# Kernel tuning notes

Hardware: AMD Instinct MI355X
Metric: run time of the kernel (lower is better)

The kernel has to match this reference:

```python
import jax, jax.numpy as jnp
import numpy as np

C_IN = 4
C_OUT = 8
K = 5            # kernel_size (hardcoded by reshape(25,2) in original)
N_ROT = 8
R_B = 8          # rot_basis_size
STRIDE = 1
PAD = 2
TWO_PI = 2.0 * np.pi
ROT_SCALE = TWO_PI / R_B


def B2(x):
    # quadratic B-spline, exactly as in the torch source
    return (-3 * (-0.5 + x) ** 2 * jnp.sign(0.5 - x)
            + (-1.5 + x) ** 2 * jnp.sign(1.5 - x)
            - 3 * (1 + 2 * x) ** 2 * jnp.sign(0.5 + x) / 4
            + (3 + 2 * x) ** 2 * jnp.sign(1.5 + x) / 4) / 4


def angle_dist(th1, th2):
    return jnp.mod(th2 - th1 + np.pi, TWO_PI) - np.pi


def make_kernel_stack(weights):
    # weights: (C_IN, R_B*K*K, C_OUT). M = K*K*R_B combined (spatial-center, rot-center) index;
    # original repeats each spatial center R_B times (np.repeat) and tiles rot centers K*K times.
    lidx = -(K // 2)
    coords = jnp.arange(lidx, K // 2 + 1, dtype=jnp.float32)
    grid = jnp.stack(jnp.meshgrid(coords, coords, indexing='ij'), axis=-1)  # (K,K,2), grid[i,j]=[i+l, j+l]
    centers_xy = jnp.repeat(grid.reshape(K * K, 2), R_B, axis=0)            # (M,2)
    rot_centers = jnp.tile(jnp.arange(R_B, dtype=jnp.float32) * ROT_SCALE, K * K)  # (M,)
    rot_sample = jnp.arange(N_ROT, dtype=jnp.float32) * (TWO_PI / N_ROT)    # (N_ROT,)

    def one_kernel(theta):
        c, s = jnp.cos(theta), jnp.sin(theta)
        x, y = grid[..., 0], grid[..., 1]
        xxs = jnp.stack([x * c - y * s, x * s + y * c], axis=-1)            # (K,K,2) rotated sample grid
        xx_diffs = centers_xy[None, None, :, :] - xxs[:, :, None, :]        # (K,K,M,2)
        xx_vals = jnp.prod(B2(xx_diffs), axis=-1)                           # (K,K,M) separable spatial spline
        rots = rot_sample + theta                                           # (N_ROT,)
        rot_vals = B2(angle_dist(rots[:, None], rot_centers[None, :]) / ROT_SCALE)  # (N_ROT,M)
        vals = xx_vals[:, :, None, :] * rot_vals[None, None, :, :]          # (K,K,N_ROT,M)
        # contract basis index m against weights -> (C_OUT, C_IN, N_ROT, K, K)
        return jnp.einsum('xyrm,imo->oirxy', vals, weights)

    ks = jax.vmap(one_kernel)(-rot_sample)  # (N_ROT, C_OUT, C_IN, N_ROT, K, K), matches torch.cat over -theta
    return ks.reshape(N_ROT * C_OUT, C_IN * N_ROT, K, K)


def setup_inputs() -> dict:
    key = jax.random.key(0)
    kx, kw = jax.random.split(key)
    X = jax.random.normal(kx, (8, C_IN, N_ROT, 256, 256), dtype=jnp.float32)
    weights = jax.random.normal(kw, (C_IN, R_B * K * K, C_OUT), dtype=jnp.float32)
    return {'X': X, 'weights': weights}


def reference(X, weights):
    ks = make_kernel_stack(weights)                       # (N_ROT*C_OUT, C_IN*N_ROT, K, K)
    B, c, d, H, W = X.shape
    Xr = X.reshape(B, c * d, H, W)
    out = jax.lax.conv_general_dilated(
        Xr, ks, window_strides=(STRIDE, STRIDE),
        padding=[(PAD, PAD), (PAD, PAD)],
        dimension_numbers=('NCHW', 'OIHW', 'NCHW'))        # (B, N_ROT*C_OUT, h, w)
    Bn, _, h, w = out.shape
    out = out.reshape(Bn, N_ROT, C_OUT, h, w).transpose(0, 2, 1, 3, 4)  # (B, C_OUT, N_ROT, h, w)
    return (TWO_PI / N_ROT) * out
```

## Files before the change

### kernel.cpp

```cpp
#include <hip/hip_runtime.h>
#include <hip/hip_fp16.h>
#include <math.h>

#define PI_F      3.14159265358979323846f
#define TWO_PI_F  6.28318530717958647692f
#define PI4_F     0.78539816339744830962f

typedef _Float16 f16x8 __attribute__((ext_vector_type(8)));
typedef float    f32x4 __attribute__((ext_vector_type(4)));

__device__ __forceinline__ float sgn(float t) {
    return (t > 0.f) ? 1.f : ((t < 0.f) ? -1.f : 0.f);
}

__device__ __forceinline__ float b2(float x) {
    float a = x - 0.5f;
    float b = x - 1.5f;
    float c = 1.f + 2.f * x;
    float d = 3.f + 2.f * x;
    return (-3.f * a * a * sgn(0.5f - x)
            + b * b * sgn(1.5f - x)
            - 0.75f * c * c * sgn(0.5f + x)
            + 0.25f * d * d * sgn(1.5f + x)) * 0.25f;
}

__global__ void build_ks_kernel(const float* __restrict__ w, __half* __restrict__ ksh) {
    int g = blockIdx.x * 256 + threadIdx.x;
    if (g >= 64 * 32 * 25) return;
    int O = g & 63;
    int rest = g >> 6;
    int t = rest % 25;
    int I = rest / 25;
    int r0 = O >> 3, o = O & 7;
    int i = I >> 3, r = I & 7;
    int x = t / 5, y = t % 5;

    float theta = -(float)r0 * PI4_F;
    float cth = cosf(theta), sth = sinf(theta);
    float fx = (float)(x - 2), fy = (float)(y - 2);
    float xc = fx * cth - fy * sth;
    float yc = fx * sth + fy * cth;

    float rotv[8];
    float rs = (float)r * PI4_F + theta;
    #pragma unroll
    for (int mr = 0; mr < 8; ++mr) {
        float v = (float)mr * PI4_F - rs + PI_F;
        float md = fmodf(v, TWO_PI_F);
        if (md < 0.f) md += TWO_PI_F;
        rotv[mr] = b2((md - PI_F) / PI4_F);
    }

    float sum = 0.f;
    for (int mx = 0; mx < 25; ++mx) {
        float cx = (float)(mx / 5 - 2);
        float cy = (float)(mx % 5 - 2);
        float bx = b2(cx - xc) * b2(cy - yc);
        if (bx != 0.f) {
            const float* wp = w + (size_t)(i * 200 + mx * 8) * 8 + o;
            #pragma unroll
            for (int mr = 0; mr < 8; ++mr)
                sum = fmaf(bx * rotv[mr], wp[mr * 8], sum);
        }
    }
    ksh[(size_t)(t * 64 + O) * 32 + I] = __float2half(sum);
}

__global__ __launch_bounds__(512, 4) void conv_kernel(const float* __restrict__ X,
                                                      const __half* __restrict__ ksh,
                                                      float* __restrict__ out) {
    __shared__ uint4 xt[720 * 5];

    int blk = blockIdx.x;
    int b = blk >> 7;
    int rem = blk & 127;
    int h0 = (rem >> 3) << 4;
    int w0 = (rem & 7) << 5;
    int tid = threadIdx.x;

    const float* Xb = X + (size_t)b * 32 * 65536;

    for (int lin = tid; lin < 2880; lin += 512) {
        int slot = lin / 720;
        int pxi = lin - slot * 720;
        int r = pxi / 36;
        int c = pxi - r * 36;
        int gh = h0 + r - 2;
        int gw = w0 + c - 2;
        union { __half h[8]; uint4 u; } pk;
        if ((unsigned)gh < 256u && (unsigned)gw < 256u) {
            const float* src = Xb + (size_t)slot * 8 * 65536 + gh * 256 + gw;
            #pragma unroll
            for (int j = 0; j < 8; ++j) pk.h[j] = __float2half(src[j * 65536]);
        } else {
            pk.u = make_uint4(0u, 0u, 0u, 0u);
        }
        xt[pxi * 5 + slot] = pk.u;
    }
    __syncthreads();

    int wave = tid >> 6;
    int lane = tid & 63;
    int lO = lane & 15;
    int ks4 = lane >> 4;

    const uint4* ksq = (const uint4*)ksh;
    int bidx = lO * 4 + ks4;

    f32x4 acc[4][4] = {};

    int baseA[4];
    #pragma unroll
    for (int q = 0; q < 4; ++q) {
        int r_q = wave * 2 + (q >> 1);
        int half_q = q & 1;
        baseA[q] = (r_q * 36 + half_q * 16 + lO) * 5 + ks4;
    }

    f16x8 Bf[2][4];
    #pragma unroll
    for (int n = 0; n < 4; ++n)
        Bf[0][n] = __builtin_bit_cast(f16x8, ksq[0 * 256 + n * 64 + bidx]);

    #pragma unroll
    for (int t = 0; t < 25; ++t) {
        const int dx = t / 5, dy = t % 5;
        const int aoff = (dx * 36 + dy) * 5;
        const int cur = t & 1, nxt = cur ^ 1;

        f16x8 Af[4];
        #pragma unroll
        for (int q = 0; q < 4; ++q)
            Af[q] = __builtin_bit_cast(f16x8, xt[baseA[q] + aoff]);

        if (t < 24) {
            #pragma unroll
            for (int n = 0; n < 4; ++n)
                Bf[nxt][n] = __builtin_bit_cast(f16x8, ksq[(t + 1) * 256 + n * 64 + bidx]);
        }

        #pragma unroll
        for (int q = 0; q < 4; ++q) {
            #pragma unroll
            for (int n = 0; n < 4; ++n)
                acc[q][n] = __builtin_amdgcn_mfma_f32_16x16x32_f16(Af[q], Bf[cur][n], acc[q][n], 0, 0, 0);
        }
    }

    #pragma unroll
    for (int q = 0; q < 4; ++q) {
        int r_q = wave * 2 + (q >> 1);
        int gh = h0 + r_q;
        int gwb = w0 + (q & 1) * 16 + ks4 * 4;
        #pragma unroll
        for (int n = 0; n < 4; ++n) {
            int O = n * 16 + lO;
            float* op = out + (((size_t)(b * 8 + (O & 7)) * 8 + (O >> 3)) << 16)
                            + gh * 256 + gwb;
            f32x4 v = acc[q][n] * PI4_F;
            *(f32x4*)op = v;
        }
    }
}

extern "C" void kernel_launch(void* const* d_in, const int* in_sizes, int n_in,
                              void* d_out, int out_size, void* d_ws, size_t ws_size,
                              hipStream_t stream) {
    const float* X = (const float*)d_in[0];
    const float* w = (const float*)d_in[1];
    float* outp = (float*)d_out;
    __half* ksh = (__half*)d_ws;

    build_ks_kernel<<<(64 * 32 * 25 + 255) / 256, 256, 0, stream>>>(w, ksh);
    conv_kernel<<<8 * 16 * 8, 512, 0, stream>>>(X, ksh, outp);
}
```

Measured before the change: 110.6 us.

## Pre-transpose input to fp16 channels-last and stream tiles via async LDS loads

Adds a pass that converts X from fp32 NCHW to an fp16 pixel-major layout with 32 channels contiguous, stored in workspace. A new conv kernel then pulls halo tiles with global_load_lds 16-byte copies, uses a zero guard buffer for padding, and double-buffers four column sub-tiles per block while raising MFMA wave priority. The intent is to replace the strided per-channel fp32 gathers with contiguous async loads overlapped with compute. The cost is an extra full read/write pass over the input and a grid of only 256 single-occupancy blocks; the old path is kept as a fallback when workspace is too small.

```diff
diff --git a/kernel.cpp b/kernel.cpp
--- a/kernel.cpp
+++ b/kernel.cpp
@@ -8,6 +8,11 @@
 
 typedef _Float16 f16x8 __attribute__((ext_vector_type(8)));
 typedef float    f32x4 __attribute__((ext_vector_type(4)));
+
+#define KS_BYTES   (25 * 64 * 32 * 2)
+#define GUARD_OFF  KS_BYTES
+#define XH_OFF     ((size_t)1 << 20)
+#define XH_BYTES   ((size_t)8 * 256 * 256 * 32 * 2)
 
 __device__ __forceinline__ float sgn(float t) {
     return (t > 0.f) ? 1.f : ((t < 0.f) ? -1.f : 0.f);
@@ -24,7 +29,9 @@
             + 0.25f * d * d * sgn(1.5f + x)) * 0.25f;
 }
 
-__global__ void build_ks_kernel(const float* __restrict__ w, __half* __restrict__ ksh) {
+__global__ void build_ks_kernel(const float* __restrict__ w, __half* __restrict__ ksh,
+                                float* __restrict__ guard) {
+    if (blockIdx.x == 0 && threadIdx.x < 16) guard[threadIdx.x] = 0.f;
     int g = blockIdx.x * 256 + threadIdx.x;
     if (g >= 64 * 32 * 25) return;
     int O = g & 63;
@@ -66,99 +73,210 @@
     ksh[(size_t)(t * 64 + O) * 32 + I] = __float2half(sum);
 }
 
-__global__ __launch_bounds__(512, 4) void conv_kernel(const float* __restrict__ X,
-                                                      const __half* __restrict__ ksh,
-                                                      float* __restrict__ out) {
+__global__ __launch_bounds__(256, 2) void hwc_kernel(const float* __restrict__ X,
+                                                     __half* __restrict__ Xh) {
+    __shared__ float tl[32 * 260];
+    int b = blockIdx.x >> 8;
+    int h = blockIdx.x & 255;
+    const float* Xb = X + ((size_t)b * 32) * 65536 + h * 256;
+    int tid = threadIdx.x;
+
+    for (int idx = tid; idx < 32 * 256; idx += 256) {
+        int c = idx >> 8;
+        int ww = idx & 255;
+        tl[c * 260 + ww] = Xb[(size_t)c * 65536 + ww];
+    }
+    __syncthreads();
+
+    uint4* dst = (uint4*)(Xh + ((size_t)(b * 65536 + h * 256 + tid)) * 32);
+    #pragma unroll
+    for (int kk = 0; kk < 4; ++kk) {
+        union { __half hh[8]; uint4 u; } pk;
+        #pragma unroll
+        for (int j = 0; j < 8; ++j)
+            pk.hh[j] = __float2half(tl[(kk * 8 + j) * 260 + tid]);
+        dst[kk] = pk.u;
+    }
+}
+
+__global__ __launch_bounds__(512, 1) void conv_hwc_kernel(const __half* __restrict__ Xh,
+                                                          const __half* __restrict__ ksh,
+                                                          const __half* __restrict__ guard,
+                                                          float* __restrict__ out) {
+    __shared__ uint4 xt[2 * 2880];
+
+    int blk = blockIdx.x;
+    int b   = blk >> 5;
+    int rem = blk & 31;
+    int h0  = (rem >> 1) << 4;
+    int w0  = (rem & 1) << 7;
+    int tid = threadIdx.x;
+    int wave = tid >> 6, lane = tid & 63;
+    int lpx = lane >> 2, slot = lane & 3;
+    int lO = lane & 15, ks4 = lane >> 4;
+    int bidx = lO * 4 + ks4;
+
+    const uint4* ksq = (const uint4*)ksh;
+    const char* Xb = (const char*)Xh + (size_t)b * (65536 * 64);
+    const char* gp = (const char*)guard;
+
+    auto stage = [&](int s, uint4* dst) {
+        int w0s = w0 + s * 32;
+        for (int j = wave; j < 45; j += 8) {
+            int px = j * 16 + lpx;
+            int r = px / 36;
+            int c = px - r * 36;
+            int gh = h0 + r - 2;
+            int gw = w0s + c - 2;
+            const char* src = ((unsigned)gh < 256u && (unsigned)gw < 256u)
+                ? Xb + ((size_t)(gh * 256 + gw)) * 64 + slot * 16
+                : gp + slot * 16;
+            __builtin_amdgcn_global_load_lds(
+                (const __attribute__((address_space(1))) void*)src,
+                (__attribute__((address_space(3))) void*)(dst + j * 64),
+                16, 0, 0);
+        }
+    };
+
+    int baseA[4];
+    #pragma unroll
+    for (int q = 0; q < 4; ++q) {
+        int r_q = wave * 2 + (q >> 1);
+        baseA[q] = (r_q * 36 + (q & 1) * 16 + lO) * 4 + ks4;
+    }
+
+    stage(0, xt);
+    asm volatile("s_waitcnt vmcnt(0)" ::: "memory");
+    __builtin_amdgcn_s_barrier();
+
+    #pragma unroll 1
+    for (int s = 0; s < 4; ++s) {
+        uint4* cbuf = xt + (s & 1) * 2880;
+        uint4* nbuf = xt + ((s & 1) ^ 1) * 2880;
+        if (s < 3) stage(s + 1, nbuf);
+
+        f32x4 acc[4][4] = {};
+        f16x8 Af[2][4], Bf[2][4];
+        #pragma unroll
+        for (int q = 0; q < 4; ++q)
+            Af[0][q] = __builtin_bit_cast(f16x8, cbuf[baseA[q]]);
+        #pragma unroll
+        for (int n = 0; n < 4; ++n)
+            Bf[0][n] = __builtin_bit_cast(f16x8, ksq[n * 64 + bidx]);
+
+        #pragma unroll
+        for (int t = 0; t < 25; ++t) {
+            const int cur = t & 1, nxt = cur ^ 1;
+            if (t < 24) {
+                const int t1 = t + 1;
+                const int aoff = ((t1 / 5) * 36 + (t1 % 5)) * 4;
+                #pragma unroll
+                for (int q = 0; q < 4; ++q)
+                    Af[nxt][q] = __builtin_bit_cast(f16x8, cbuf[baseA[q] + aoff]);
+                #pragma unroll
+                for (int n = 0; n < 4; ++n)
+                    Bf[nxt][n] = __builtin_bit_cast(f16x8, ksq[t1 * 256 + n * 64 + bidx]);
+            }
+            __builtin_amdgcn_s_setprio(1);
+            #pragma unroll
+            for (int q = 0; q < 4; ++q) {
+                #pragma unroll
+                for (int n = 0; n < 4; ++n)
+                    acc[q][n] = __builtin_amdgcn_mfma_f32_16x16x32_f16(Af[cur][q], Bf[cur][n], acc[q][n], 0, 0, 0);
+            }
+            __builtin_amdgcn_s_setprio(0);
+        }
+
+        int w0s = w0 + s * 32;
+        #pragma unroll
+        for (int q = 0; q < 4; ++q) {
+            int gh  = h0 + wave * 2 + (q >> 1);
+            int gwb = w0s + (q & 1) * 16 + ks4 * 4;
+            #pragma unroll
+            for (int n = 0; n < 4; ++n) {
+                int O = n * 16 + lO;
+                float* op = out + (((size_t)(b * 8 + (O & 7)) * 8 + (O >> 3)) << 16)
+                                + gh * 256 + gwb;
+                *(f32x4*)op = acc[q][n] * PI4_F;
+            }
+        }
+
+        if (s < 3) {
+            asm volatile("s_waitcnt vmcnt(16) lgkmcnt(0)" ::: "memory");
+            __builtin_amdgcn_s_barrier();
+        }
+    }
+}
+
+__global__ __launch_bounds__(512, 4) void conv_kernel_f32(const float* __restrict__ X,
+                                                          const __half* __restrict__ ksh,
+                                                          float* __restrict__ out) {
     __shared__ uint4 xt[720 * 5];
-
     int blk = blockIdx.x;
     int b = blk >> 7;
     int rem = blk & 127;
     int h0 = (rem >> 3) << 4;
     int w0 = (rem & 7) << 5;
     int tid = threadIdx.x;
-
     const float* Xb = X + (size_t)b * 32 * 65536;
-
     for (int lin = tid; lin < 2880; lin += 512) {
-        int slot = lin / 720;
-        int pxi = lin - slot * 720;
+        int slotq = lin / 720;
+        int pxi = lin - slotq * 720;
         int r = pxi / 36;
         int c = pxi - r * 36;
         int gh = h0 + r - 2;
         int gw = w0 + c - 2;
         union { __half h[8]; uint4 u; } pk;
         if ((unsigned)gh < 256u && (unsigned)gw < 256u) {
-            const float* src = Xb + (size_t)slot * 8 * 65536 + gh * 256 + gw;
+            const float* src = Xb + (size_t)slotq * 8 * 65536 + gh * 256 + gw;
             #pragma unroll
             for (int j = 0; j < 8; ++j) pk.h[j] = __float2half(src[j * 65536]);
         } else {
             pk.u = make_uint4(0u, 0u, 0u, 0u);
         }
-        xt[pxi * 5 + slot] = pk.u;
+        xt[pxi * 5 + slotq] = pk.u;
     }
     __syncthreads();
-
-    int wave = tid >> 6;
-    int lane = tid & 63;
-    int lO = lane & 15;
-    int ks4 = lane >> 4;
-
+    int wave = tid >> 6, lane = tid & 63;
+    int lO = lane & 15, ks4 = lane >> 4;
     const uint4* ksq = (const uint4*)ksh;
     int bidx = lO * 4 + ks4;
-
     f32x4 acc[4][4] = {};
-
     int baseA[4];
     #pragma unroll
-    for (int q = 0; q < 4; ++q) {
-        int r_q = wave * 2 + (q >> 1);
-        int half_q = q & 1;
-        baseA[q] = (r_q * 36 + half_q * 16 + lO) * 5 + ks4;
-    }
-
+    for (int q = 0; q < 4; ++q)
+        baseA[q] = ((wave * 2 + (q >> 1)) * 36 + (q & 1) * 16 + lO) * 5 + ks4;
     f16x8 Bf[2][4];
     #pragma unroll
     for (int n = 0; n < 4; ++n)
-        Bf[0][n] = __builtin_bit_cast(f16x8, ksq[0 * 256 + n * 64 + bidx]);
-
+        Bf[0][n] = __builtin_bit_cast(f16x8, ksq[n * 64 + bidx]);
     #pragma unroll
     for (int t = 0; t < 25; ++t) {
-        const int dx = t / 5, dy = t % 5;
-        const int aoff = (dx * 36 + dy) * 5;
         const int cur = t & 1, nxt = cur ^ 1;
-
         f16x8 Af[4];
         #pragma unroll
         for (int q = 0; q < 4; ++q)
-            Af[q] = __builtin_bit_cast(f16x8, xt[baseA[q] + aoff]);
-
+            Af[q] = __builtin_bit_cast(f16x8, xt[baseA[q] + ((t / 5) * 36 + (t % 5)) * 5]);
         if (t < 24) {
             #pragma unroll
             for (int n = 0; n < 4; ++n)
                 Bf[nxt][n] = __builtin_bit_cast(f16x8, ksq[(t + 1) * 256 + n * 64 + bidx]);
         }
-
-        #pragma unroll
-        for (int q = 0; q < 4; ++q) {
+        #pragma unroll
+        for (int q = 0; q < 4; ++q)
             #pragma unroll
             for (int n = 0; n < 4; ++n)
                 acc[q][n] = __builtin_amdgcn_mfma_f32_16x16x32_f16(Af[q], Bf[cur][n], acc[q][n], 0, 0, 0);
-        }
-    }
-
+    }
     #pragma unroll
     for (int q = 0; q < 4; ++q) {
-        int r_q = wave * 2 + (q >> 1);
-        int gh = h0 + r_q;
+        int gh = h0 + wave * 2 + (q >> 1);
         int gwb = w0 + (q & 1) * 16 + ks4 * 4;
         #pragma unroll
         for (int n = 0; n < 4; ++n) {
             int O = n * 16 + lO;
-            float* op = out + (((size_t)(b * 8 + (O & 7)) * 8 + (O >> 3)) << 16)
-                            + gh * 256 + gwb;
-            f32x4 v = acc[q][n] * PI4_F;
-            *(f32x4*)op = v;
+            float* op = out + (((size_t)(b * 8 + (O & 7)) * 8 + (O >> 3)) << 16) + gh * 256 + gwb;
+            *(f32x4*)op = acc[q][n] * PI4_F;
         }
     }
 }
@@ -169,8 +287,17 @@
     const float* X = (const float*)d_in[0];
     const float* w = (const float*)d_in[1];
     float* outp = (float*)d_out;
-    __half* ksh = (__half*)d_ws;
-
-    build_ks_kernel<<<(64 * 32 * 25 + 255) / 256, 256, 0, stream>>>(w, ksh);
-    conv_kernel<<<8 * 16 * 8, 512, 0, stream>>>(X, ksh, outp);
-}
+    char* ws = (char*)d_ws;
+    __half* ksh = (__half*)ws;
+    float* guard = (float*)(ws + GUARD_OFF);
+
+    build_ks_kernel<<<(64 * 32 * 25 + 255) / 256, 256, 0, stream>>>(w, ksh, guard);
+
+    if (ws_size >= XH_OFF + XH_BYTES) {
+        __half* Xh = (__half*)(ws + XH_OFF);
+        hwc_kernel<<<8 * 256, 256, 0, stream>>>(X, Xh);
+        conv_hwc_kernel<<<256, 512, 0, stream>>>(Xh, ksh, (const __half*)guard, outp);
+    } else {
+        conv_kernel_f32<<<8 * 16 * 8, 512, 0, stream>>>(X, ksh, outp);
+    }
+}
```

Result: slower. 216.3 us (+95.6%).

## Enlarge conv tile to 32x32 pixels with slot-major padded LDS layout

Applied to the files above, without the earlier changes.

Doubles the output tile per block from 16x32 to 32x32 pixels, so each wave computes 8 MFMA row-tiles instead of 4. This halves the halo overhead and gives more reuse of each kernel-weight fragment loaded per tap. The shared-memory layout changes from pixel-interleaved to slot-major with a padded stride of 1297 to avoid bank conflicts. MFMA sections are wrapped in s_setprio. The costs are a larger LDS footprint, more accumulator registers, lower occupancy (launch bounds 2), and only 512 blocks on the device.

```diff
diff --git a/kernel.cpp b/kernel.cpp
--- a/kernel.cpp
+++ b/kernel.cpp
@@ -66,99 +66,91 @@
     ksh[(size_t)(t * 64 + O) * 32 + I] = __float2half(sum);
 }
 
-__global__ __launch_bounds__(512, 4) void conv_kernel(const float* __restrict__ X,
-                                                      const __half* __restrict__ ksh,
-                                                      float* __restrict__ out) {
-    __shared__ uint4 xt[720 * 5];
+__global__ __launch_bounds__(512, 2) void conv_fused_kernel(const float* __restrict__ X,
+                                                            const __half* __restrict__ ksh,
+                                                            float* __restrict__ out) {
+    __shared__ uint4 xt[4 * 1297];
 
-    int blk = blockIdx.x;
-    int b = blk >> 7;
-    int rem = blk & 127;
-    int h0 = (rem >> 3) << 4;
-    int w0 = (rem & 7) << 5;
+    int bid = blockIdx.x;
+    int b   = bid >> 6;
+    int rem = bid & 63;
+    int h0  = (rem >> 3) << 5;
+    int w0  = (rem & 7) << 5;
     int tid = threadIdx.x;
 
     const float* Xb = X + (size_t)b * 32 * 65536;
 
-    for (int lin = tid; lin < 2880; lin += 512) {
-        int slot = lin / 720;
-        int pxi = lin - slot * 720;
-        int r = pxi / 36;
-        int c = pxi - r * 36;
+    for (int lin = tid; lin < 4 * 1296; lin += 512) {
+        int slot = lin / 1296;
+        int p    = lin - slot * 1296;
+        int r = p / 36, c = p - (p / 36) * 36;
         int gh = h0 + r - 2;
         int gw = w0 + c - 2;
-        union { __half h[8]; uint4 u; } pk;
+        union { __half hh[8]; uint4 u; } pk;
         if ((unsigned)gh < 256u && (unsigned)gw < 256u) {
             const float* src = Xb + (size_t)slot * 8 * 65536 + gh * 256 + gw;
             #pragma unroll
-            for (int j = 0; j < 8; ++j) pk.h[j] = __float2half(src[j * 65536]);
+            for (int j = 0; j < 8; ++j) pk.hh[j] = __float2half(src[j * 65536]);
         } else {
             pk.u = make_uint4(0u, 0u, 0u, 0u);
         }
-        xt[pxi * 5 + slot] = pk.u;
+        xt[slot * 1297 + p] = pk.u;
     }
     __syncthreads();
 
-    int wave = tid >> 6;
-    int lane = tid & 63;
-    int lO = lane & 15;
-    int ks4 = lane >> 4;
+    int wave = tid >> 6, lane = tid & 63;
+    int lO = lane & 15, ks4 = lane >> 4;
+    int bidx = lO * 4 + ks4;
+    const uint4* ksq = (const uint4*)ksh;
 
-    const uint4* ksq = (const uint4*)ksh;
-    int bidx = lO * 4 + ks4;
-
-    f32x4 acc[4][4] = {};
-
-    int baseA[4];
+    f32x4 acc[8][4] = {};
+    int baseA[8];
     #pragma unroll
-    for (int q = 0; q < 4; ++q) {
-        int r_q = wave * 2 + (q >> 1);
-        int half_q = q & 1;
-        baseA[q] = (r_q * 36 + half_q * 16 + lO) * 5 + ks4;
-    }
+    for (int m = 0; m < 8; ++m)
+        baseA[m] = 1297 * ks4 + (wave * 4 + (m >> 1)) * 36 + (m & 1) * 16 + lO;
 
     f16x8 Bf[2][4];
     #pragma unroll
     for (int n = 0; n < 4; ++n)
-        Bf[0][n] = __builtin_bit_cast(f16x8, ksq[0 * 256 + n * 64 + bidx]);
+        Bf[0][n] = __builtin_bit_cast(f16x8, ksq[n * 64 + bidx]);
 
     #pragma unroll
     for (int t = 0; t < 25; ++t) {
-        const int dx = t / 5, dy = t % 5;
-        const int aoff = (dx * 36 + dy) * 5;
         const int cur = t & 1, nxt = cur ^ 1;
+        const int aoff = (t / 5) * 36 + (t % 5);
 
-        f16x8 Af[4];
+        f16x8 Af[8];
         #pragma unroll
-        for (int q = 0; q < 4; ++q)
-            Af[q] = __builtin_bit_cast(f16x8, xt[baseA[q] + aoff]);
+        for (int m = 0; m < 8; ++m)
+            Af[m] = __builtin_bit_cast(f16x8, xt[baseA[m] + aoff]);
 
         if (t < 24) {
+            const int t1 = t + 1;
             #pragma unroll
             for (int n = 0; n < 4; ++n)
-                Bf[nxt][n] = __builtin_bit_cast(f16x8, ksq[(t + 1) * 256 + n * 64 + bidx]);
+                Bf[nxt][n] = __builtin_bit_cast(f16x8, ksq[t1 * 256 + n * 64 + bidx]);
         }
 
+        __builtin_amdgcn_s_setprio(1);
         #pragma unroll
-        for (int q = 0; q < 4; ++q) {
+        for (int m = 0; m < 8; ++m) {
             #pragma unroll
             for (int n = 0; n < 4; ++n)
-                acc[q][n] = __builtin_amdgcn_mfma_f32_16x16x32_f16(Af[q], Bf[cur][n], acc[q][n], 0, 0, 0);
+                acc[m][n] = __builtin_amdgcn_mfma_f32_16x16x32_f16(Af[m], Bf[cur][n], acc[m][n], 0, 0, 0);
         }
+        __builtin_amdgcn_s_setprio(0);
     }
 
     #pragma unroll
-    for (int q = 0; q < 4; ++q) {
-        int r_q = wave * 2 + (q >> 1);
-        int gh = h0 + r_q;
-        int gwb = w0 + (q & 1) * 16 + ks4 * 4;
+    for (int m = 0; m < 8; ++m) {
+        int gh  = h0 + wave * 4 + (m >> 1);
+        int gwb = w0 + (m & 1) * 16 + ks4 * 4;
         #pragma unroll
         for (int n = 0; n < 4; ++n) {
             int O = n * 16 + lO;
             float* op = out + (((size_t)(b * 8 + (O & 7)) * 8 + (O >> 3)) << 16)
                             + gh * 256 + gwb;
-            f32x4 v = acc[q][n] * PI4_F;
-            *(f32x4*)op = v;
+            *(f32x4*)op = acc[m][n] * PI4_F;
         }
     }
 }
@@ -171,6 +163,6 @@
     float* outp = (float*)d_out;
     __half* ksh = (__half*)d_ws;
 
-    build_ks_kernel<<<(64 * 32 * 25 + 255) / 256, 256, 0, stream>>>(w, ksh);
-    conv_kernel<<<8 * 16 * 8, 512, 0, stream>>>(X, ksh, outp);
+    build_ks_kernel<<<200, 256, 0, stream>>>(w, ksh);
+    conv_fused_kernel<<<8 * 64, 512, 0, stream>>>(X, ksh, outp);
 }
```

Result: faster. 98.36 us (-11.1%).
